# Kernel optimization log

Hardware: AMD Instinct MI355X
Metric: run time of the kernel (lower is better)

## Reference

```python
import jax, jax.numpy as jnp
import numpy as np

B, S, D_IN, D_OUT, H = 2, 2048, 1024, 1024, 16
HD = D_OUT // H  # head dim = 64


def setup_inputs() -> dict:
    key = jax.random.key(0)
    ks = jax.random.split(key, 9)
    s_in = 1.0 / np.sqrt(D_IN)
    s_out = 1.0 / np.sqrt(D_OUT)
    return {
        "X": jax.random.normal(ks[0], (B, S, D_IN), dtype=jnp.float32),
        "Wq": jax.random.uniform(ks[1], (D_OUT, D_IN), jnp.float32, -s_in, s_in),
        "bq": jax.random.uniform(ks[2], (D_OUT,), jnp.float32, -s_in, s_in),
        "Wk": jax.random.uniform(ks[3], (D_OUT, D_IN), jnp.float32, -s_in, s_in),
        "bk": jax.random.uniform(ks[4], (D_OUT,), jnp.float32, -s_in, s_in),
        "Wv": jax.random.uniform(ks[5], (D_OUT, D_IN), jnp.float32, -s_in, s_in),
        "bv": jax.random.uniform(ks[6], (D_OUT,), jnp.float32, -s_in, s_in),
        "Wo": jax.random.uniform(ks[7], (D_OUT, D_OUT), jnp.float32, -s_out, s_out),
        "bo": jax.random.uniform(ks[8], (D_OUT,), jnp.float32, -s_out, s_out),
    }


def reference(X, Wq, bq, Wk, bk, Wv, bv, Wo, bo):
    scale = jnp.asarray(HD ** 0.5, X.dtype)  # self.dim = sqrt(head_dim)
    q = X @ Wq.T + bq  # [B,S,D_OUT]
    k = X @ Wk.T + bk
    v = X @ Wv.T + bv
    # split heads: b s (h d) -> b h s d
    q = q.reshape(B, S, H, HD).transpose(0, 2, 1, 3)
    k = k.reshape(B, S, H, HD).transpose(0, 2, 1, 3)
    v = v.reshape(B, S, H, HD).transpose(0, 2, 1, 3)
    scores = jnp.einsum('bhsd,bhtd->bhst', q, k) / scale  # [B,H,S,S]
    causal = jnp.triu(jnp.ones((S, S), dtype=bool), k=1)
    scores = jnp.where(causal, -jnp.inf, scores)
    weights = jax.nn.softmax(scores, axis=-1)
    out = jnp.einsum('bhst,bhtd->bhsd', weights, v)  # [B,H,S,HD]
    out = out.transpose(0, 2, 1, 3).reshape(B, S, D_OUT)  # b h s d -> b s (h d)
    return out @ Wo.T + bo
```

## Files before the change

kernel.cpp:

```cpp
#include <hip/hip_runtime.h>
#include <hip/hip_bf16.h>

typedef __bf16 bf16_t;
typedef __bf16 bf16x8 __attribute__((ext_vector_type(8)));
typedef float  f32x4  __attribute__((ext_vector_type(4)));
typedef unsigned short ushort_t;

#define MFMA16(a, b, c) __builtin_amdgcn_mfma_f32_16x16x32_bf16((a), (b), (c), 0, 0, 0)
#define GLDS16(g, l) __builtin_amdgcn_global_load_lds( \
    (const __attribute__((address_space(1))) unsigned int*)(g), \
    (__attribute__((address_space(3))) unsigned int*)(l), 16, 0, 0)

#define WAITCNT_VM(n)  (0x0F70 | (n))
#define WAITCNT_LGKM0  0xC07F


__global__ __launch_bounds__(256) void cvt_all(
    const void* __restrict__ X,  const void* __restrict__ W0, const void* __restrict__ W1,
    const void* __restrict__ W2, const void* __restrict__ W3,
    const void* __restrict__ c0, const void* __restrict__ c1,
    const void* __restrict__ c2, const void* __restrict__ c3,
    bf16_t* __restrict__ Xb, bf16_t* __restrict__ Wb, float* __restrict__ biasF,
    int* __restrict__ flag)
{
    const int tid  = threadIdx.x;
    const int lane = tid & 63;
    const ushort_t u = ((const ushort_t*)X)[2 * lane];
    const int e = (u >> 7) & 0xFF;
    const int f = (__ballot(e >= 0xA0) != 0ull) ? 1 : 0;

    const int bid = blockIdx.x;
    if (bid >= 4096) {
        if (bid == 4096 && tid == 0) *flag = f;
        const int idx = ((bid - 4096) * 256 + tid) * 8;
        const int w = idx >> 10, off = idx & 1023;
        const void* src = (w == 0) ? c0 : (w == 1) ? c1 : (w == 2) ? c2 : c3;
        #pragma unroll
        for (int r = 0; r < 8; ++r)
            biasF[idx + r] = f ? ((const float*)src)[off + r]
                               : (float)((const bf16_t*)src)[off + r];
        return;
    }

    const long long i = (long long)bid * 2048 + tid * 8;
    const void* src;
    bf16_t* dst;
    long long off;
    if (i < 4194304) { src = X; dst = Xb; off = i; }
    else {
        const int w = (int)((i - 4194304) >> 20);
        off = (i - 4194304) & 1048575;
        src = (w == 0) ? W0 : (w == 1) ? W1 : (w == 2) ? W2 : W3;
        dst = Wb + (size_t)w * 1048576;
    }
    if (f) {
        const float* s = (const float*)src + off;
        const float4 a = *(const float4*)(s);
        const float4 b = *(const float4*)(s + 4);
        bf16x8 o;
        o[0] = (bf16_t)a.x; o[1] = (bf16_t)a.y; o[2] = (bf16_t)a.z; o[3] = (bf16_t)a.w;
        o[4] = (bf16_t)b.x; o[5] = (bf16_t)b.y; o[6] = (bf16_t)b.z; o[7] = (bf16_t)b.w;
        *(bf16x8*)(dst + off) = o;
    } else {
        *(bf16x8*)(dst + off) = *(const bf16x8*)((const bf16_t*)src + off);
    }
}

template<int TM>
__global__ __launch_bounds__(256, 2) void gemm_nt(
    const bf16_t* __restrict__ A,
    const bf16_t* __restrict__ W0, const bf16_t* __restrict__ W1, const bf16_t* __restrict__ W2,
    const float* __restrict__ b0, const float* __restrict__ b1, const float* __restrict__ b2,
    void* __restrict__ C, int ldc, bf16_t* __restrict__ Vt, int fuse_vt,
    const int* __restrict__ flag, int is_out)
{
    constexpr int MI = TM / 32;
    constexpr int G  = (TM == 128) ? 4 : 3;
    __shared__ bf16_t Ash[3][TM * 32];
    __shared__ bf16_t Bsh[3][128 * 32];

    const int f32out = is_out ? *flag : 0;

    const int tid  = threadIdx.x;
    const int wid  = tid >> 6;
    const int lane = tid & 63;
    const int g    = lane >> 4;
    const int c    = lane & 15;

    const int m0  = blockIdx.x * TM;
    const int n0  = blockIdx.y * 128;
    const int mat = n0 >> 10;
    const bf16_t* W  = (mat == 0) ? W0 : (mat == 1) ? W1 : W2;
    const float*  bs = (mat == 0) ? b0 : (mat == 1) ? b1 : b2;
    const int nw = n0 & 1023;

    const int srow = lane >> 2;
    const int sblk = (lane & 3) ^ ((lane >> 3) & 3);
    const bf16_t* Ag = A + (size_t)(m0 + wid * (TM / 4) + srow) * 1024 + sblk * 8;
    const bf16_t* Wg = W + (size_t)(nw + wid * 32 + srow) * 1024 + sblk * 8;

    const int waveM = (wid >> 1) * (TM / 2);
    const int waveN = (wid & 1) * 64;

    f32x4 acc[MI][4] = {};
    const int fblk = (g ^ ((c >> 1) & 3)) * 8;

    auto stage = [&](int t, int buf) {
        const int k0 = t * 32;
        bf16_t* As = &Ash[buf][(wid * (TM / 4)) * 32];
        bf16_t* Bs = &Bsh[buf][(wid * 32) * 32];
        GLDS16(Ag + k0, As);
        if (TM == 128) GLDS16(Ag + (size_t)16 * 1024 + k0, As + 16 * 32);
        GLDS16(Wg + k0, Bs);
        GLDS16(Wg + (size_t)16 * 1024 + k0, Bs + 16 * 32);
    };

    stage(0, 0);
    stage(1, 1);

    #pragma unroll 3
    for (int k = 0; k < 32; ++k) {
        if (k < 30) {
            stage(k + 2, (k + 2) % 3);
            __builtin_amdgcn_s_waitcnt(WAITCNT_VM(2 * G));
        } else if (k == 30) {
            __builtin_amdgcn_s_waitcnt(WAITCNT_VM(G));
        } else {
            __builtin_amdgcn_s_waitcnt(WAITCNT_VM(0));
        }
        __builtin_amdgcn_s_barrier();
        asm volatile("" ::: "memory");

        const int cur = k % 3;
        bf16x8 af[MI], bfr[4];
        #pragma unroll
        for (int i = 0; i < MI; ++i)
            af[i] = *(const bf16x8*)(&Ash[cur][(waveM + i * 16 + c) * 32 + fblk]);
        #pragma unroll
        for (int j = 0; j < 4; ++j)
            bfr[j] = *(const bf16x8*)(&Bsh[cur][(waveN + j * 16 + c) * 32 + fblk]);
        #pragma unroll
        for (int i = 0; i < MI; ++i)
            #pragma unroll
            for (int j = 0; j < 4; ++j)
                acc[i][j] = MFMA16(af[i], bfr[j], acc[i][j]);

        asm volatile("" ::: "memory");
        __builtin_amdgcn_s_waitcnt(WAITCNT_LGKM0);
        __builtin_amdgcn_s_barrier();
    }

    if (fuse_vt && mat == 2) {
        #pragma unroll
        for (int j = 0; j < 4; ++j) {
            const int col  = n0 + waveN + j * 16 + c;
            const int hcol = col & 1023;
            const float bv = bs[hcol];
            const int h = hcol >> 6, d = hcol & 63;
            #pragma unroll
            for (int i = 0; i < MI; ++i) {
                const int row = m0 + waveM + i * 16 + g * 4;
                const int bb = row >> 11, s = row & 2047;
                bf16_t pk[4];
                #pragma unroll
                for (int r = 0; r < 4; ++r) pk[r] = (bf16_t)(acc[i][j][r] + bv);
                *(uint2*)(&Vt[(((size_t)bb * 16 + h) * 64 + d) * 2048 + s]) = *(uint2*)pk;
            }
        }
        return;
    }

    #pragma unroll
    for (int j = 0; j < 4; ++j) {
        const int col = n0 + waveN + j * 16 + c;
        const float bv = bs[col & 1023];
        #pragma unroll
        for (int i = 0; i < MI; ++i) {
            const int row = m0 + waveM + i * 16 + g * 4;
            #pragma unroll
            for (int r = 0; r < 4; ++r) {
                const float val = acc[i][j][r] + bv;
                const size_t idx = (size_t)(row + r) * ldc + col;
                if (f32out) ((float*)C)[idx] = val;
                else        ((bf16_t*)C)[idx] = (bf16_t)val;
            }
        }
    }
}

__global__ __launch_bounds__(256, 2) void attn_kernel(
    const bf16_t* __restrict__ QKV, const bf16_t* __restrict__ Vt,
    bf16_t* __restrict__ O)
{
    __shared__ bf16_t Ksh[64][72];
    __shared__ bf16_t Vsh[64][72];
    __shared__ bf16_t Psh[4][32][72];

    const int tid  = threadIdx.x;
    const int wid  = tid >> 6;
    const int lane = tid & 63;
    const int g    = lane >> 4;
    const int c    = lane & 15;

    const int bh = blockIdx.y;
    const int b  = bh >> 4, h = bh & 15;
    const int qt = (bh < 16) ? blockIdx.x : (15 - blockIdx.x);
    const int q0 = qt * 128;
    const int nt = 2 * qt + 2;

    bf16x8 aq[2][2];
    #pragma unroll
    for (int qf = 0; qf < 2; ++qf) {
        const bf16_t* qp = QKV + (size_t)(b * 2048 + q0 + wid * 32 + qf * 16 + c) * 3072 + h * 64;
        #pragma unroll
        for (int kb = 0; kb < 2; ++kb) {
            bf16x8 t = *(const bf16x8*)(qp + kb * 32 + g * 8);
            #pragma unroll
            for (int j = 0; j < 8; ++j) t[j] = (bf16_t)((float)t[j] * 0.125f);
            aq[qf][kb] = t;
        }
    }

    float li[2][4] = {};
    f32x4 o[2][4]  = {};

    const int sr  = tid >> 2;
    const int sc0 = (tid & 3) * 16;
    const bf16_t* Kg = QKV + (size_t)(b * 2048 + sr) * 3072 + 1024 + h * 64 + sc0;
    const bf16_t* Vg = Vt + ((size_t)bh * 64 + sr) * 2048 + sc0;

    uint4 kr0 = *(const uint4*)(Kg);
    uint4 kr1 = *(const uint4*)(Kg + 8);
    uint4 vr0 = *(const uint4*)(Vg);
    uint4 vr1 = *(const uint4*)(Vg + 8);

    for (int jt = 0; jt < nt; ++jt) {
        *(uint4*)(&Ksh[sr][sc0])     = kr0;
        *(uint4*)(&Ksh[sr][sc0 + 8]) = kr1;
        *(uint4*)(&Vsh[sr][sc0])     = vr0;
        *(uint4*)(&Vsh[sr][sc0 + 8]) = vr1;
        __syncthreads();

        if (jt + 1 < nt) {
            const size_t ko = (size_t)(jt + 1) * 64 * 3072;
            kr0 = *(const uint4*)(Kg + ko);
            kr1 = *(const uint4*)(Kg + ko + 8);
            vr0 = *(const uint4*)(Vg + (jt + 1) * 64);
            vr1 = *(const uint4*)(Vg + (jt + 1) * 64 + 8);
        }

        f32x4 s[2][4] = {};
        #pragma unroll
        for (int n = 0; n < 4; ++n)
            #pragma unroll
            for (int kb = 0; kb < 2; ++kb) {
                const bf16x8 kf = *(const bf16x8*)(&Ksh[n * 16 + c][kb * 32 + g * 8]);
                s[0][n] = MFMA16(aq[0][kb], kf, s[0][n]);
                s[1][n] = MFMA16(aq[1][kb], kf, s[1][n]);
            }

        if (jt >= nt - 2) {
            const int j0 = jt * 64;
            #pragma unroll
            for (int qf = 0; qf < 2; ++qf) {
                const int qrow = q0 + wid * 32 + qf * 16 + g * 4;
                #pragma unroll
                for (int n = 0; n < 4; ++n)
                    #pragma unroll
                    for (int r = 0; r < 4; ++r)
                        if (j0 + n * 16 + c > qrow + r) s[qf][n][r] = -1e30f;
            }
        }

        #pragma unroll
        for (int qf = 0; qf < 2; ++qf)
            #pragma unroll
            for (int n = 0; n < 4; ++n)
                #pragma unroll
                for (int r = 0; r < 4; ++r) {
                    const float p = __expf(s[qf][n][r]);
                    li[qf][r] += p;
                    Psh[wid][qf * 16 + g * 4 + r][n * 16 + c] = (bf16_t)p;
                }
        __builtin_amdgcn_wave_barrier();

        #pragma unroll
        for (int kb = 0; kb < 2; ++kb) {
            const bf16x8 ap0 = *(const bf16x8*)(&Psh[wid][c][kb * 32 + g * 8]);
            const bf16x8 ap1 = *(const bf16x8*)(&Psh[wid][16 + c][kb * 32 + g * 8]);
            #pragma unroll
            for (int d = 0; d < 4; ++d) {
                const bf16x8 vf = *(const bf16x8*)(&Vsh[d * 16 + c][kb * 32 + g * 8]);
                o[0][d] = MFMA16(ap0, vf, o[0][d]);
                o[1][d] = MFMA16(ap1, vf, o[1][d]);
            }
        }
        __syncthreads();
    }

    #pragma unroll
    for (int off = 1; off < 16; off <<= 1)
        #pragma unroll
        for (int qf = 0; qf < 2; ++qf)
            #pragma unroll
            for (int r = 0; r < 4; ++r)
                li[qf][r] += __shfl_xor(li[qf][r], off, 64);

    #pragma unroll
    for (int qf = 0; qf < 2; ++qf) {
        const int orow = b * 2048 + q0 + wid * 32 + qf * 16 + g * 4;
        #pragma unroll
        for (int r = 0; r < 4; ++r) {
            const float inv = 1.0f / li[qf][r];
            #pragma unroll
            for (int d = 0; d < 4; ++d)
                O[(size_t)(orow + r) * 1024 + h * 64 + d * 16 + c] = (bf16_t)(o[qf][d][r] * inv);
        }
    }
}

extern "C" void kernel_launch(void* const* d_in, const int* in_sizes, int n_in,
                              void* d_out, int out_size, void* d_ws, size_t ws_size,
                              hipStream_t stream)
{
    const void* X  = d_in[0];
    const void* Wq = d_in[1];  const void* bq = d_in[2];
    const void* Wk = d_in[3];  const void* bk = d_in[4];
    const void* Wv = d_in[5];  const void* bv = d_in[6];
    const void* Wo = d_in[7];  const void* bo = d_in[8];

    int*    flag  = (int*)d_ws;
    float*  biasF = (float*)((char*)d_ws + 16);
    bf16_t* Xb    = (bf16_t*)((char*)d_ws + 16 + 16384);
    bf16_t* Wb    = Xb  + (size_t)4096 * 1024;
    bf16_t* QKV   = Wb  + (size_t)4 * 1024 * 1024;
    bf16_t* Vt    = QKV + (size_t)4096 * 3072;
    bf16_t* Ao    = Vt  + (size_t)4096 * 1024;

    const size_t MW = (size_t)1024 * 1024;

    cvt_all<<<4098, 256, 0, stream>>>(X, Wq, Wk, Wv, Wo, bq, bk, bv, bo,
                                      Xb, Wb, biasF, flag);

    gemm_nt<64><<<dim3(64, 24), 256, 0, stream>>>(
        Xb, Wb, Wb + MW, Wb + 2 * MW,
        biasF, biasF + 1024, biasF + 2048, QKV, 3072, Vt, 1, flag, 0);
    attn_kernel<<<dim3(16, 32), 256, 0, stream>>>(QKV, Vt, Ao);
    gemm_nt<64><<<dim3(64, 8), 256, 0, stream>>>(
        Ao, Wb + 3 * MW, Wb + 3 * MW, Wb + 3 * MW,
        biasF + 3072, biasF + 3072, biasF + 3072, d_out, 1024, (bf16_t*)nullptr, 0, flag, 1);
}
```

Before: 226.1 us.

## Shrink attention query tile to 64 rows, use exp2 softmax, enlarge QKV GEMM tile

Attention blocks now cover 64 query rows (16 per wave) instead of 128. This doubles the grid, halves the per-block LDS and register footprint, and raises the launch-bounds occupancy hint to 4. The exponent switches to a hardware exp2 with the log2(e) factor folded into the Q prescale. Causal masking now applies only on the last diagonal tile. The QKV projection GEMM moves to a 128-row tile with half as many blocks. The trade-off is more blocks each reloading K/V, and less MFMA work per K/V tile loaded into LDS.

```diff
diff --git a/kernel.cpp b/kernel.cpp
--- a/kernel.cpp
+++ b/kernel.cpp
@@ -188,13 +188,13 @@
     }
 }
 
-__global__ __launch_bounds__(256, 2) void attn_kernel(
+__global__ __launch_bounds__(256, 4) void attn_kernel(
     const bf16_t* __restrict__ QKV, const bf16_t* __restrict__ Vt,
     bf16_t* __restrict__ O)
 {
     __shared__ bf16_t Ksh[64][72];
     __shared__ bf16_t Vsh[64][72];
-    __shared__ bf16_t Psh[4][32][72];
+    __shared__ bf16_t Psh[4][16][72];
 
     const int tid  = threadIdx.x;
     const int wid  = tid >> 6;
@@ -204,25 +204,24 @@
 
     const int bh = blockIdx.y;
     const int b  = bh >> 4, h = bh & 15;
-    const int qt = (bh < 16) ? blockIdx.x : (15 - blockIdx.x);
-    const int q0 = qt * 128;
-    const int nt = 2 * qt + 2;
-
-    bf16x8 aq[2][2];
-    #pragma unroll
-    for (int qf = 0; qf < 2; ++qf) {
-        const bf16_t* qp = QKV + (size_t)(b * 2048 + q0 + wid * 32 + qf * 16 + c) * 3072 + h * 64;
+    const int qt = (bh < 16) ? blockIdx.x : (31 - blockIdx.x);
+    const int q0 = qt * 64;
+    const int nt = qt + 1;
+
+    bf16x8 aq[2];
+    {
+        const bf16_t* qp = QKV + (size_t)(b * 2048 + q0 + wid * 16 + c) * 3072 + h * 64;
         #pragma unroll
         for (int kb = 0; kb < 2; ++kb) {
             bf16x8 t = *(const bf16x8*)(qp + kb * 32 + g * 8);
             #pragma unroll
-            for (int j = 0; j < 8; ++j) t[j] = (bf16_t)((float)t[j] * 0.125f);
-            aq[qf][kb] = t;
-        }
-    }
-
-    float li[2][4] = {};
-    f32x4 o[2][4]  = {};
+            for (int j = 0; j < 8; ++j) t[j] = (bf16_t)((float)t[j] * 0.18033688f);
+            aq[kb] = t;
+        }
+    }
+
+    float li[4] = {};
+    f32x4 o[4]  = {};
 
     const int sr  = tid >> 2;
     const int sc0 = (tid & 3) * 16;
@@ -249,50 +248,42 @@
             vr1 = *(const uint4*)(Vg + (jt + 1) * 64 + 8);
         }
 
-        f32x4 s[2][4] = {};
+        f32x4 s[4] = {};
         #pragma unroll
         for (int n = 0; n < 4; ++n)
             #pragma unroll
             for (int kb = 0; kb < 2; ++kb) {
                 const bf16x8 kf = *(const bf16x8*)(&Ksh[n * 16 + c][kb * 32 + g * 8]);
-                s[0][n] = MFMA16(aq[0][kb], kf, s[0][n]);
-                s[1][n] = MFMA16(aq[1][kb], kf, s[1][n]);
-            }
-
-        if (jt >= nt - 2) {
+                s[n] = MFMA16(aq[kb], kf, s[n]);
+            }
+
+        if (jt == nt - 1) {
             const int j0 = jt * 64;
-            #pragma unroll
-            for (int qf = 0; qf < 2; ++qf) {
-                const int qrow = q0 + wid * 32 + qf * 16 + g * 4;
-                #pragma unroll
-                for (int n = 0; n < 4; ++n)
-                    #pragma unroll
-                    for (int r = 0; r < 4; ++r)
-                        if (j0 + n * 16 + c > qrow + r) s[qf][n][r] = -1e30f;
-            }
-        }
-
-        #pragma unroll
-        for (int qf = 0; qf < 2; ++qf)
+            const int qrow = q0 + wid * 16 + g * 4;
             #pragma unroll
             for (int n = 0; n < 4; ++n)
                 #pragma unroll
-                for (int r = 0; r < 4; ++r) {
-                    const float p = __expf(s[qf][n][r]);
-                    li[qf][r] += p;
-                    Psh[wid][qf * 16 + g * 4 + r][n * 16 + c] = (bf16_t)p;
-                }
+                for (int r = 0; r < 4; ++r)
+                    if (j0 + n * 16 + c > qrow + r) s[n][r] = -1e30f;
+        }
+
+        #pragma unroll
+        for (int n = 0; n < 4; ++n)
+            #pragma unroll
+            for (int r = 0; r < 4; ++r) {
+                const float p = __builtin_amdgcn_exp2f(s[n][r]);
+                li[r] += p;
+                Psh[wid][g * 4 + r][n * 16 + c] = (bf16_t)p;
+            }
         __builtin_amdgcn_wave_barrier();
 
         #pragma unroll
         for (int kb = 0; kb < 2; ++kb) {
-            const bf16x8 ap0 = *(const bf16x8*)(&Psh[wid][c][kb * 32 + g * 8]);
-            const bf16x8 ap1 = *(const bf16x8*)(&Psh[wid][16 + c][kb * 32 + g * 8]);
+            const bf16x8 ap = *(const bf16x8*)(&Psh[wid][c][kb * 32 + g * 8]);
             #pragma unroll
             for (int d = 0; d < 4; ++d) {
                 const bf16x8 vf = *(const bf16x8*)(&Vsh[d * 16 + c][kb * 32 + g * 8]);
-                o[0][d] = MFMA16(ap0, vf, o[0][d]);
-                o[1][d] = MFMA16(ap1, vf, o[1][d]);
+                o[d] = MFMA16(ap, vf, o[d]);
             }
         }
         __syncthreads();
@@ -301,21 +292,16 @@
     #pragma unroll
     for (int off = 1; off < 16; off <<= 1)
         #pragma unroll
-        for (int qf = 0; qf < 2; ++qf)
-            #pragma unroll
-            for (int r = 0; r < 4; ++r)
-                li[qf][r] += __shfl_xor(li[qf][r], off, 64);
-
+        for (int r = 0; r < 4; ++r)
+            li[r] += __shfl_xor(li[r], off, 64);
+
+    const int orow = b * 2048 + q0 + wid * 16 + g * 4;
     #pragma unroll
-    for (int qf = 0; qf < 2; ++qf) {
-        const int orow = b * 2048 + q0 + wid * 32 + qf * 16 + g * 4;
-        #pragma unroll
-        for (int r = 0; r < 4; ++r) {
-            const float inv = 1.0f / li[qf][r];
-            #pragma unroll
-            for (int d = 0; d < 4; ++d)
-                O[(size_t)(orow + r) * 1024 + h * 64 + d * 16 + c] = (bf16_t)(o[qf][d][r] * inv);
-        }
+    for (int r = 0; r < 4; ++r) {
+        const float inv = 1.0f / li[r];
+        #pragma unroll
+        for (int d = 0; d < 4; ++d)
+            O[(size_t)(orow + r) * 1024 + h * 64 + d * 16 + c] = (bf16_t)(o[d][r] * inv);
     }
 }
 
@@ -342,10 +328,10 @@
     cvt_all<<<4098, 256, 0, stream>>>(X, Wq, Wk, Wv, Wo, bq, bk, bv, bo,
                                       Xb, Wb, biasF, flag);
 
-    gemm_nt<64><<<dim3(64, 24), 256, 0, stream>>>(
+    gemm_nt<128><<<dim3(32, 24), 256, 0, stream>>>(
         Xb, Wb, Wb + MW, Wb + 2 * MW,
         biasF, biasF + 1024, biasF + 2048, QKV, 3072, Vt, 1, flag, 0);
-    attn_kernel<<<dim3(16, 32), 256, 0, stream>>>(QKV, Vt, Ao);
+    attn_kernel<<<dim3(32, 32), 256, 0, stream>>>(QKV, Vt, Ao);
     gemm_nt<64><<<dim3(64, 8), 256, 0, stream>>>(
         Ao, Wb + 3 * MW, Wb + 3 * MW, Wb + 3 * MW,
         biasF + 3072, biasF + 3072, biasF + 3072, d_out, 1024, (bf16_t*)nullptr, 0, flag, 1);
```

Result: faster. 201.9 us (-10.7%).
